# Kernel optimization log

Hardware: AMD Instinct MI355X
Metric: run time of the kernel (lower is better)

The kernel has to match this reference:

```python
import jax, jax.numpy as jnp
import numpy as np

N, F, DE = 768, 64, 32
H0, H1, H2, OUT = 64, 64, 128, 1  # hidden_dim=[64,64,128], output_dim=1


def _mlp(x, Wa, ba, Wb, bb):
    # two Dense layers with relu, as in the repo's MLP
    h = jax.nn.relu(x @ Wa + ba)
    return jax.nn.relu(h @ Wb + bb)


def _edge_conv_e(A, x, e, Wa, ba, Wb, bb):
    # EdgeConvE: per-edge message MLP([x_i, x_j - x_i, e_ij]) aggregated
    # over neighbors j weighted by the (binary) adjacency.
    n = x.shape[0]
    xi = jnp.broadcast_to(x[:, None, :], (n, n, x.shape[1]))  # [N,N,F]
    xj = jnp.broadcast_to(x[None, :, :], (n, n, x.shape[1]))  # [N,N,F]
    feat = jnp.concatenate([xi, xj - xi, e], axis=-1)         # [N,N,2F+De]
    m = _mlp(feat, Wa, ba, Wb, bb)                            # [N,N,H]
    return jnp.einsum('ij,ijh->ih', A, m)                     # scatter-sum over j


def setup_inputs() -> dict:
    key = jax.random.key(0)
    ks = jax.random.split(key, 16)
    adj = (jax.random.uniform(ks[0], (N, N)) < 0.05).astype(jnp.float32)
    x = jax.random.normal(ks[1], (N, F), dtype=jnp.float32)
    e = jax.random.normal(ks[2], (N, N, DE), dtype=jnp.float32)
    s = 0.05
    d_in1 = 2 * F + DE          # 160
    d_in2 = 2 * H0 + DE         # 160
    return {
        'ajacency': adj,
        'node_features': x,
        'edge_attributes': e,
        'W1a': jax.random.normal(ks[3], (d_in1, H0)) * s, 'b1a': jnp.zeros((H0,)),
        'W1b': jax.random.normal(ks[4], (H0, H0)) * s,    'b1b': jnp.zeros((H0,)),
        'W2a': jax.random.normal(ks[5], (d_in2, H1)) * s, 'b2a': jnp.zeros((H1,)),
        'W2b': jax.random.normal(ks[6], (H1, H0)) * s,    'b2b': jnp.zeros((H0,)),
        'W3': jax.random.normal(ks[7], (H0, H2)) * s,     'b3': jnp.zeros((H2,)),
        'W4': jax.random.normal(ks[8], (H2, OUT)) * s,    'b4': jnp.zeros((OUT,)),
    }


def reference(ajacency, node_features, edge_attributes,
              W1a, b1a, W1b, b1b, W2a, b2a, W2b, b2b, W3, b3, W4, b4):
    x = _edge_conv_e(ajacency, node_features, edge_attributes, W1a, b1a, W1b, b1b)
    x = _edge_conv_e(ajacency, x, edge_attributes, W2a, b2a, W2b, b2b)
    x = jax.nn.relu(x @ W3 + b3)
    return jax.nn.sigmoid(x @ W4 + b4)  # [N, OUT]
```

## Files before the change

### kernel.cpp

```cpp
#include <hip/hip_runtime.h>
#include <math.h>


#define NN 768
#define FF 64
#define DE 32
#define HH 64
#define EPB 16
#define MAXB 8
#define CAP 128
#define SH1S 72

using bf16x8 = __attribute__((ext_vector_type(8))) short;
using f32x4  = __attribute__((ext_vector_type(4))) float;

__device__ __forceinline__ short f2b(float f) {
  unsigned u = __float_as_uint(f);
  return (short)((u + 0x7fffu + ((u >> 16) & 1u)) >> 16);
}

__global__ __launch_bounds__(256) void scan_kernel(
    const float* __restrict__ A, const float* __restrict__ x,
    const float* __restrict__ e,
    const float* __restrict__ W, const float* __restrict__ bias,
    const float* __restrict__ We1, const float* __restrict__ We2,
    const float* __restrict__ Wb1, const float* __restrict__ Wb2,
    int* __restrict__ cnt, int* __restrict__ jl,
    float* __restrict__ U, float* __restrict__ V,
    float* __restrict__ ew1, float* __restrict__ ew2,
    short* __restrict__ Wbp1, short* __restrict__ Wbp2)
{
  const int i = blockIdx.x;
  const int tid = threadIdx.x;
  __shared__ int s_cnt;
  __shared__ int s_j[CAP];
  __shared__ float sx[64];
  __shared__ float su[4][64], sv[4][64];
  __shared__ __align__(16) float es[CAP][DE];

  if (tid == 0) s_cnt = 0;
  __syncthreads();
  if (tid < 64) sx[tid] = x[i * 64 + tid];
  if (tid < NN / 4) {
    float4 a = ((const float4*)(A + i * NN))[tid];
    if (a.x != 0.0f) { int p = atomicAdd(&s_cnt, 1); if (p < CAP) s_j[p] = tid * 4 + 0; }
    if (a.y != 0.0f) { int p = atomicAdd(&s_cnt, 1); if (p < CAP) s_j[p] = tid * 4 + 1; }
    if (a.z != 0.0f) { int p = atomicAdd(&s_cnt, 1); if (p < CAP) s_j[p] = tid * 4 + 2; }
    if (a.w != 0.0f) { int p = atomicAdd(&s_cnt, 1); if (p < CAP) s_j[p] = tid * 4 + 3; }
  }
  __syncthreads();
  const int c = min(s_cnt, CAP);

  for (int slot = tid >> 3; slot < c; slot += 32) {
    const int j = s_j[slot];
    ((float4*)es[slot])[tid & 7] =
        ((const float4*)(e + ((size_t)i * NN + j) * DE))[tid & 7];
  }

  const int c64 = tid & 63, sg = tid >> 6;
  float w1[DE], w2[DE];
#pragma unroll
  for (int d = 0; d < DE; ++d) { w1[d] = We1[d * HH + c64]; w2[d] = We2[d * HH + c64]; }
  __syncthreads();

  for (int slot = sg; slot < c; slot += 4) {
    float a1 = 0.0f, a2 = 0.0f;
#pragma unroll
    for (int d = 0; d < DE; ++d) {
      const float f = es[slot][d];
      a1 = fmaf(f, w1[d], a1);
      a2 = fmaf(f, w2[d], a2);
    }
    ew1[((size_t)(i << 7) + slot) * HH + c64] = a1;
    ew2[((size_t)(i << 7) + slot) * HH + c64] = a2;
  }

  {
    float u = 0.0f, v = 0.0f;
#pragma unroll
    for (int t = 0; t < 16; ++t) {
      const int d = sg * 16 + t;
      const float xv = sx[d];
      const float wxi = W[d * 64 + c64];
      const float wxj = W[(64 + d) * 64 + c64];
      u = fmaf(xv, wxi - wxj, u);
      v = fmaf(xv, wxj, v);
    }
    su[sg][c64] = u; sv[sg][c64] = v;
  }

  if (i < 2) {
    const float* src = (i == 0) ? Wb1 : Wb2;
    short* dst = (i == 0) ? Wbp1 : Wbp2;
    for (int L = tid; L < 4096; L += 256) {
      const int j = L & 7, n = (L >> 3) & 15, quad = (L >> 7) & 3;
      const int kb = (L >> 9) & 1, ct = L >> 10;
      dst[L] = f2b(src[(kb * 32 + quad * 8 + j) * 64 + ct * 16 + n]);
    }
  }
  __syncthreads();

  if (tid < 64) {
    U[i * 64 + tid] = su[0][tid] + su[1][tid] + su[2][tid] + su[3][tid] + bias[tid];
    V[i * 64 + tid] = sv[0][tid] + sv[1][tid] + sv[2][tid] + sv[3][tid];
  }
  if (tid == 0) cnt[i] = c;
  for (int t = tid; t < c; t += 256) jl[(i << 7) + t] = s_j[t];
}

__global__ __launch_bounds__(256) void conv_kernel(
    const int* __restrict__ cnt, const int* __restrict__ jl,
    const float* __restrict__ U, const float* __restrict__ V,
    const float* __restrict__ ew, const short* __restrict__ Wbp,
    const float* __restrict__ bb, float* __restrict__ xp)
{
  const int i = blockIdx.x >> 3;
  const int chunk = blockIdx.x & (MAXB - 1);
  const int t0 = chunk * EPB;
  const int c = cnt[i];
  if (t0 >= c) return;
  const int nedge = min(EPB, c - t0);

  const int tid = threadIdx.x, lane = tid & 63, wv = tid >> 6;
  __shared__ __align__(16) short sh1b[EPB * SH1S];

  const float u_i = U[(i << 6) + lane];
#pragma unroll
  for (int t = 0; t < 4; ++t) {
    const int slot = wv * 4 + t;
    const int idx = t0 + (slot < nedge ? slot : nedge - 1);
    const int j = jl[(i << 7) + idx];
    const float h = u_i + V[(j << 6) + lane]
                  + ew[((size_t)(i << 7) + idx) * HH + lane];
    sh1b[slot * SH1S + lane] = f2b(fmaxf(h, 0.0f));
  }
  __syncthreads();

  const int q = lane >> 4, n = lane & 15;
  bf16x8 b0 = *(const bf16x8*)(Wbp + (((wv * 2 + 0) * 4 + q) * 16 + n) * 8);
  bf16x8 b1 = *(const bf16x8*)(Wbp + (((wv * 2 + 1) * 4 + q) * 16 + n) * 8);
  const float bias = bb[wv * 16 + n];
  const short* sa = sh1b + n * SH1S + q * 8;
  bf16x8 a0 = *(const bf16x8*)(sa);
  bf16x8 a1 = *(const bf16x8*)(sa + 32);

  f32x4 acc = {0.f, 0.f, 0.f, 0.f};
  acc = __builtin_amdgcn_mfma_f32_16x16x32_bf16(a0, b0, acc, 0, 0, 0);
  acc = __builtin_amdgcn_mfma_f32_16x16x32_bf16(a1, b1, acc, 0, 0, 0);

  float s = 0.0f;
#pragma unroll
  for (int reg = 0; reg < 4; ++reg) {
    const int row = q * 4 + reg;
    const float v = fmaxf(acc[reg] + bias, 0.0f);
    s += (row < nedge) ? v : 0.0f;
  }
  s += __shfl_down(s, 32);
  s += __shfl_down(s, 16);
  if (lane < 16)
    xp[(((i << 3) + chunk) << 6) + wv * 16 + lane] = s;
}

__global__ __launch_bounds__(256, 4) void uv2_kernel(
    const int* __restrict__ cnt, const float* __restrict__ xp,
    const float* __restrict__ W, const float* __restrict__ bias,
    float* __restrict__ U, float* __restrict__ V)
{
  const int tid = threadIdx.x;
  const int rr = tid >> 6, c64 = tid & 63;
  const int r = blockIdx.x * 4 + rr;
  __shared__ float sx[4][64];
  const int nch = (cnt[r] + EPB - 1) / EPB;
  float xv = 0.0f;
  for (int ch = 0; ch < nch; ++ch) xv += xp[(((r << 3) + ch) << 6) + c64];
  sx[rr][c64] = xv;
  __syncthreads();
  float u = bias[c64], v = 0.0f;
#pragma unroll
  for (int d = 0; d < 64; ++d) {
    const float t = sx[rr][d];
    const float wxi = W[d * 64 + c64];
    const float wxj = W[(64 + d) * 64 + c64];
    u = fmaf(t, wxi - wxj, u);
    v = fmaf(t, wxj, v);
  }
  U[r * 64 + c64] = u;
  V[r * 64 + c64] = v;
}

__global__ __launch_bounds__(128) void final_kernel(
    const int* __restrict__ cnt, const float* __restrict__ xp,
    const float* __restrict__ W3, const float* __restrict__ b3,
    const float* __restrict__ W4, const float* __restrict__ b4,
    float* __restrict__ out)
{
  const int i = blockIdx.x;
  const int t = threadIdx.x;
  const int lane = t & 63;
  const int wv = t >> 6;
  __shared__ float sx[64];
  __shared__ float s_red[2];
  if (t < 64) {
    const int nch = (cnt[i] + EPB - 1) / EPB;
    float xv = 0.0f;
    for (int ch = 0; ch < nch; ++ch) xv += xp[(((i << 3) + ch) << 6) + t];
    sx[t] = xv;
  }
  __syncthreads();
  float p = b3[t];
#pragma unroll
  for (int c = 0; c < 64; ++c) p = fmaf(sx[c], W3[c * 128 + t], p);
  p = fmaxf(p, 0.0f);
  float v = p * W4[t];
  v += __shfl_down(v, 32);
  v += __shfl_down(v, 16);
  v += __shfl_down(v, 8);
  v += __shfl_down(v, 4);
  v += __shfl_down(v, 2);
  v += __shfl_down(v, 1);
  if (lane == 0) s_red[wv] = v;
  __syncthreads();
  if (t == 0) {
    float z = s_red[0] + s_red[1] + b4[0];
    out[i] = 1.0f / (1.0f + expf(-z));
  }
}

extern "C" void kernel_launch(void* const* d_in, const int* in_sizes, int n_in,
                              void* d_out, int out_size, void* d_ws, size_t ws_size,
                              hipStream_t stream) {
  const float* A   = (const float*)d_in[0];
  const float* x   = (const float*)d_in[1];
  const float* e   = (const float*)d_in[2];
  const float* W1a = (const float*)d_in[3];
  const float* b1a = (const float*)d_in[4];
  const float* W1b = (const float*)d_in[5];
  const float* b1b = (const float*)d_in[6];
  const float* W2a = (const float*)d_in[7];
  const float* b2a = (const float*)d_in[8];
  const float* W2b = (const float*)d_in[9];
  const float* b2b = (const float*)d_in[10];
  const float* W3  = (const float*)d_in[11];
  const float* b3  = (const float*)d_in[12];
  const float* W4  = (const float*)d_in[13];
  const float* b4  = (const float*)d_in[14];
  float* out = (float*)d_out;

  int*   cnt  = (int*)d_ws;
  int*   jl   = cnt + NN;
  float* U1   = (float*)(jl + NN * CAP);
  float* V1   = U1 + NN * HH;
  float* U2   = V1 + NN * HH;
  float* V2   = U2 + NN * HH;
  float* ew1  = V2 + NN * HH;
  float* ew2  = ew1 + (size_t)NN * CAP * HH;
  float* x1p  = ew2 + (size_t)NN * CAP * HH;
  float* x2p  = x1p + NN * MAXB * HH;
  short* Wbp1 = (short*)(x2p + NN * MAXB * HH);
  short* Wbp2 = Wbp1 + 4096;

  scan_kernel<<<NN, 256, 0, stream>>>(A, x, e, W1a, b1a,
                                      W1a + 128 * HH, W2a + 128 * HH,
                                      W1b, W2b,
                                      cnt, jl, U1, V1, ew1, ew2, Wbp1, Wbp2);
  conv_kernel<<<NN * MAXB, 256, 0, stream>>>(cnt, jl, U1, V1, ew1, Wbp1, b1b, x1p);
  uv2_kernel<<<NN / 4, 256, 0, stream>>>(cnt, x1p, W2a, b2a, U2, V2);
  conv_kernel<<<NN * MAXB, 256, 0, stream>>>(cnt, jl, U2, V2, ew2, Wbp2, b2b, x2p);
  final_kernel<<<NN, 128, 0, stream>>>(cnt, x2p, W3, b3, W4, b4, out);
}
```

Baseline: 162.3 us.

## Fuse conv with uv2 and head into per-node blocks, drop partial-sum buffers

Each node now gets a single block that loops over all its edges in 16-row MFMA tiles, replacing the split into up to 8 chunk blocks per node. The layer-1 conv is fused with the U2/V2 projection, and the layer-2 conv is fused with the MLP head. This cuts the launch count from five to three and removes the x1p/x2p partial-sum round trips through global memory. In exchange there is less parallelism per node (768 blocks instead of up to 6144), each block loops serially over edge tiles, and shared memory per block grows to about 18KB.

```diff
diff --git a/kernel.cpp b/kernel.cpp
--- a/kernel.cpp
+++ b/kernel.cpp
@@ -6,8 +6,6 @@
 #define FF 64
 #define DE 32
 #define HH 64
-#define EPB 16
-#define MAXB 8
 #define CAP 128
 #define SH1S 72
 
@@ -108,120 +106,131 @@
   for (int t = tid; t < c; t += 256) jl[(i << 7) + t] = s_j[t];
 }
 
-__global__ __launch_bounds__(256) void conv_kernel(
-    const int* __restrict__ cnt, const int* __restrict__ jl,
+__device__ __forceinline__ void conv_body(
+    int i, int c, const int* __restrict__ jl,
     const float* __restrict__ U, const float* __restrict__ V,
     const float* __restrict__ ew, const short* __restrict__ Wbp,
-    const float* __restrict__ bb, float* __restrict__ xp)
-{
-  const int i = blockIdx.x >> 3;
-  const int chunk = blockIdx.x & (MAXB - 1);
-  const int t0 = chunk * EPB;
-  const int c = cnt[i];
-  if (t0 >= c) return;
-  const int nedge = min(EPB, c - t0);
-
+    const float* __restrict__ bb, short* sh1b, float* xrow,
+    int tid, int lane, int wv)
+{
+  const int nt = (c + 15) >> 4;
+  const int cpad = nt << 4;
+
+  if (c > 0) {
+    const float u_i = U[(i << 6) + lane];
+    for (int slot = wv; slot < cpad; slot += 4) {
+      short val = 0;
+      if (slot < c) {
+        const int j = jl[(i << 7) + slot];
+        const float h = u_i + V[(j << 6) + lane]
+                      + ew[((size_t)(i << 7) + slot) * HH + lane];
+        val = f2b(fmaxf(h, 0.0f));
+      }
+      sh1b[slot * SH1S + lane] = val;
+    }
+  }
+  __syncthreads();
+
+  if (c > 0) {
+    const int q = lane >> 4, n = lane & 15;
+    bf16x8 b0 = *(const bf16x8*)(Wbp + (((wv * 2 + 0) * 4 + q) * 16 + n) * 8);
+    bf16x8 b1 = *(const bf16x8*)(Wbp + (((wv * 2 + 1) * 4 + q) * 16 + n) * 8);
+    const float bias = bb[wv * 16 + n];
+    float s = 0.0f;
+    for (int rt = 0; rt < nt; ++rt) {
+      const short* sa = sh1b + (rt * 16 + n) * SH1S + q * 8;
+      bf16x8 a0 = *(const bf16x8*)(sa);
+      bf16x8 a1 = *(const bf16x8*)(sa + 32);
+      f32x4 acc = {0.f, 0.f, 0.f, 0.f};
+      acc = __builtin_amdgcn_mfma_f32_16x16x32_bf16(a0, b0, acc, 0, 0, 0);
+      acc = __builtin_amdgcn_mfma_f32_16x16x32_bf16(a1, b1, acc, 0, 0, 0);
+#pragma unroll
+      for (int reg = 0; reg < 4; ++reg) {
+        const int row = rt * 16 + q * 4 + reg;
+        const float v = fmaxf(acc[reg] + bias, 0.0f);
+        s += (row < c) ? v : 0.0f;
+      }
+    }
+    s += __shfl_down(s, 32);
+    s += __shfl_down(s, 16);
+    if (lane < 16) xrow[wv * 16 + lane] = s;
+  } else {
+    if (lane < 16) xrow[wv * 16 + lane] = 0.0f;
+  }
+  __syncthreads();
+}
+
+__global__ __launch_bounds__(256) void conv1uv2_kernel(
+    const int* __restrict__ cnt, const int* __restrict__ jl,
+    const float* __restrict__ U1, const float* __restrict__ V1,
+    const float* __restrict__ ew1, const short* __restrict__ Wbp1,
+    const float* __restrict__ b1b,
+    const float* __restrict__ W2a, const float* __restrict__ b2a,
+    float* __restrict__ U2, float* __restrict__ V2)
+{
+  const int i = blockIdx.x;
   const int tid = threadIdx.x, lane = tid & 63, wv = tid >> 6;
-  __shared__ __align__(16) short sh1b[EPB * SH1S];
-
-  const float u_i = U[(i << 6) + lane];
-#pragma unroll
-  for (int t = 0; t < 4; ++t) {
-    const int slot = wv * 4 + t;
-    const int idx = t0 + (slot < nedge ? slot : nedge - 1);
-    const int j = jl[(i << 7) + idx];
-    const float h = u_i + V[(j << 6) + lane]
-                  + ew[((size_t)(i << 7) + idx) * HH + lane];
-    sh1b[slot * SH1S + lane] = f2b(fmaxf(h, 0.0f));
-  }
-  __syncthreads();
-
-  const int q = lane >> 4, n = lane & 15;
-  bf16x8 b0 = *(const bf16x8*)(Wbp + (((wv * 2 + 0) * 4 + q) * 16 + n) * 8);
-  bf16x8 b1 = *(const bf16x8*)(Wbp + (((wv * 2 + 1) * 4 + q) * 16 + n) * 8);
-  const float bias = bb[wv * 16 + n];
-  const short* sa = sh1b + n * SH1S + q * 8;
-  bf16x8 a0 = *(const bf16x8*)(sa);
-  bf16x8 a1 = *(const bf16x8*)(sa + 32);
-
-  f32x4 acc = {0.f, 0.f, 0.f, 0.f};
-  acc = __builtin_amdgcn_mfma_f32_16x16x32_bf16(a0, b0, acc, 0, 0, 0);
-  acc = __builtin_amdgcn_mfma_f32_16x16x32_bf16(a1, b1, acc, 0, 0, 0);
-
-  float s = 0.0f;
-#pragma unroll
-  for (int reg = 0; reg < 4; ++reg) {
-    const int row = q * 4 + reg;
-    const float v = fmaxf(acc[reg] + bias, 0.0f);
-    s += (row < nedge) ? v : 0.0f;
-  }
-  s += __shfl_down(s, 32);
-  s += __shfl_down(s, 16);
-  if (lane < 16)
-    xp[(((i << 3) + chunk) << 6) + wv * 16 + lane] = s;
-}
-
-__global__ __launch_bounds__(256, 4) void uv2_kernel(
-    const int* __restrict__ cnt, const float* __restrict__ xp,
-    const float* __restrict__ W, const float* __restrict__ bias,
-    float* __restrict__ U, float* __restrict__ V)
-{
-  const int tid = threadIdx.x;
-  const int rr = tid >> 6, c64 = tid & 63;
-  const int r = blockIdx.x * 4 + rr;
-  __shared__ float sx[4][64];
-  const int nch = (cnt[r] + EPB - 1) / EPB;
-  float xv = 0.0f;
-  for (int ch = 0; ch < nch; ++ch) xv += xp[(((r << 3) + ch) << 6) + c64];
-  sx[rr][c64] = xv;
-  __syncthreads();
-  float u = bias[c64], v = 0.0f;
-#pragma unroll
-  for (int d = 0; d < 64; ++d) {
-    const float t = sx[rr][d];
-    const float wxi = W[d * 64 + c64];
-    const float wxj = W[(64 + d) * 64 + c64];
-    u = fmaf(t, wxi - wxj, u);
-    v = fmaf(t, wxj, v);
-  }
-  U[r * 64 + c64] = u;
-  V[r * 64 + c64] = v;
-}
-
-__global__ __launch_bounds__(128) void final_kernel(
-    const int* __restrict__ cnt, const float* __restrict__ xp,
+  __shared__ __align__(16) short sh1b[CAP * SH1S];
+  __shared__ float xrow[64];
+  __shared__ float su[4][64], sv[4][64];
+
+  conv_body(i, cnt[i], jl, U1, V1, ew1, Wbp1, b1b, sh1b, xrow, tid, lane, wv);
+
+  const int c64 = tid & 63, qr = tid >> 6;
+  {
+    float u = 0.0f, v = 0.0f;
+#pragma unroll
+    for (int t = 0; t < 16; ++t) {
+      const int d = qr * 16 + t;
+      const float xv = xrow[d];
+      const float wxi = W2a[d * 64 + c64];
+      const float wxj = W2a[(64 + d) * 64 + c64];
+      u = fmaf(xv, wxi - wxj, u);
+      v = fmaf(xv, wxj, v);
+    }
+    su[qr][c64] = u; sv[qr][c64] = v;
+  }
+  __syncthreads();
+  if (tid < 64) {
+    U2[i * 64 + tid] = su[0][tid] + su[1][tid] + su[2][tid] + su[3][tid] + b2a[tid];
+    V2[i * 64 + tid] = sv[0][tid] + sv[1][tid] + sv[2][tid] + sv[3][tid];
+  }
+}
+
+__global__ __launch_bounds__(256) void conv2head_kernel(
+    const int* __restrict__ cnt, const int* __restrict__ jl,
+    const float* __restrict__ U2, const float* __restrict__ V2,
+    const float* __restrict__ ew2, const short* __restrict__ Wbp2,
+    const float* __restrict__ b2b,
     const float* __restrict__ W3, const float* __restrict__ b3,
     const float* __restrict__ W4, const float* __restrict__ b4,
     float* __restrict__ out)
 {
   const int i = blockIdx.x;
-  const int t = threadIdx.x;
-  const int lane = t & 63;
-  const int wv = t >> 6;
-  __shared__ float sx[64];
-  __shared__ float s_red[2];
-  if (t < 64) {
-    const int nch = (cnt[i] + EPB - 1) / EPB;
-    float xv = 0.0f;
-    for (int ch = 0; ch < nch; ++ch) xv += xp[(((i << 3) + ch) << 6) + t];
-    sx[t] = xv;
-  }
-  __syncthreads();
-  float p = b3[t];
-#pragma unroll
-  for (int c = 0; c < 64; ++c) p = fmaf(sx[c], W3[c * 128 + t], p);
-  p = fmaxf(p, 0.0f);
-  float v = p * W4[t];
-  v += __shfl_down(v, 32);
-  v += __shfl_down(v, 16);
-  v += __shfl_down(v, 8);
-  v += __shfl_down(v, 4);
-  v += __shfl_down(v, 2);
-  v += __shfl_down(v, 1);
-  if (lane == 0) s_red[wv] = v;
-  __syncthreads();
-  if (t == 0) {
-    float z = s_red[0] + s_red[1] + b4[0];
+  const int tid = threadIdx.x, lane = tid & 63, wv = tid >> 6;
+  __shared__ __align__(16) short sh1b[CAP * SH1S];
+  __shared__ float xrow[64];
+  __shared__ float sred[2];
+
+  conv_body(i, cnt[i], jl, U2, V2, ew2, Wbp2, b2b, sh1b, xrow, tid, lane, wv);
+
+  if (tid < 128) {
+    float p = b3[tid];
+#pragma unroll
+    for (int c = 0; c < 64; ++c) p = fmaf(xrow[c], W3[c * 128 + tid], p);
+    p = fmaxf(p, 0.0f);
+    float v = p * W4[tid];
+    v += __shfl_down(v, 32);
+    v += __shfl_down(v, 16);
+    v += __shfl_down(v, 8);
+    v += __shfl_down(v, 4);
+    v += __shfl_down(v, 2);
+    v += __shfl_down(v, 1);
+    if (lane == 0) sred[wv] = v;
+  }
+  __syncthreads();
+  if (tid == 0) {
+    const float z = sred[0] + sred[1] + b4[0];
     out[i] = 1.0f / (1.0f + expf(-z));
   }
 }
@@ -254,17 +263,15 @@
   float* V2   = U2 + NN * HH;
   float* ew1  = V2 + NN * HH;
   float* ew2  = ew1 + (size_t)NN * CAP * HH;
-  float* x1p  = ew2 + (size_t)NN * CAP * HH;
-  float* x2p  = x1p + NN * MAXB * HH;
-  short* Wbp1 = (short*)(x2p + NN * MAXB * HH);
+  short* Wbp1 = (short*)(ew2 + (size_t)NN * CAP * HH);
   short* Wbp2 = Wbp1 + 4096;
 
   scan_kernel<<<NN, 256, 0, stream>>>(A, x, e, W1a, b1a,
                                       W1a + 128 * HH, W2a + 128 * HH,
                                       W1b, W2b,
                                       cnt, jl, U1, V1, ew1, ew2, Wbp1, Wbp2);
-  conv_kernel<<<NN * MAXB, 256, 0, stream>>>(cnt, jl, U1, V1, ew1, Wbp1, b1b, x1p);
-  uv2_kernel<<<NN / 4, 256, 0, stream>>>(cnt, x1p, W2a, b2a, U2, V2);
-  conv_kernel<<<NN * MAXB, 256, 0, stream>>>(cnt, jl, U2, V2, ew2, Wbp2, b2b, x2p);
-  final_kernel<<<NN, 128, 0, stream>>>(cnt, x2p, W3, b3, W4, b4, out);
-}
+  conv1uv2_kernel<<<NN, 256, 0, stream>>>(cnt, jl, U1, V1, ew1, Wbp1, b1b,
+                                          W2a, b2a, U2, V2);
+  conv2head_kernel<<<NN, 256, 0, stream>>>(cnt, jl, U2, V2, ew2, Wbp2, b2b,
+                                           W3, b3, W4, b4, out);
+}
```

New measurement: 163.2 us. About the same (+0.5%).
